# Optimization experiments

Measured on AMD Instinct MI355X. Metric: run time of the kernel, lower is better.

Reference implementation:

```python
import jax, jax.numpy as jnp
import numpy as np

B, S, DEC, ENC, ATTN = 64, 1024, 1024, 1024, 1024

def setup_inputs() -> dict:
    key = jax.random.key(0)
    k1, k2, k3, k4, k5 = jax.random.split(key, 5)
    hidden = jax.random.normal(k1, (B, DEC), dtype=jnp.float32)
    encoder_outputs = jax.random.normal(k2, (B, S, ENC), dtype=jnp.float32)
    # nn.Linear(dec+enc -> attn_dim): weight [attn, dec+enc], bias [attn]
    fan_in = DEC + ENC
    bound = 1.0 / np.sqrt(fan_in)
    W_attn = jax.random.uniform(k3, (ATTN, fan_in), dtype=jnp.float32, minval=-bound, maxval=bound)
    b_attn = jax.random.uniform(k4, (ATTN,), dtype=jnp.float32, minval=-bound, maxval=bound)
    # v = torch.rand(attn_dim) -> uniform [0,1)
    v = jax.random.uniform(k5, (ATTN,), dtype=jnp.float32)
    return {"hidden": hidden, "encoder_outputs": encoder_outputs,
            "W_attn": W_attn, "b_attn": b_attn, "v": v}

def reference(hidden, encoder_outputs, W_attn, b_attn, v):
    # hidden: [B, DEC], encoder_outputs: [B, S, ENC]
    b, s, _ = encoder_outputs.shape
    h = jnp.broadcast_to(hidden[:, None, :], (b, s, hidden.shape[-1]))
    combined = jnp.concatenate([h, encoder_outputs], axis=-1)        # [B, S, DEC+ENC]
    energy = jnp.tanh(jnp.einsum('bsf,af->bsa', combined, W_attn) + b_attn)  # [B, S, ATTN]
    scores = jnp.einsum('bsa,a->bs', energy, v)                      # [B, S]
    attn_weights = jax.nn.softmax(scores, axis=1)                    # [B, S]
    context = jnp.einsum('bs,bse->be', attn_weights, encoder_outputs)[:, None, :]  # [B, 1, ENC]
    return context
```

## Files before the change

### kernel.cpp

```cpp
#include <hip/hip_runtime.h>
#include <hip/hip_bf16.h>
#include <stdint.h>

#define NB 64
#define NS 1024
#define NE 1024
#define NA 1024
#define NF 2048
#define LDP 144

typedef __attribute__((ext_vector_type(8))) short   short8;
typedef __attribute__((ext_vector_type(4))) short   short4v;
typedef __attribute__((ext_vector_type(4))) float   f32x4;
typedef __attribute__((ext_vector_type(8))) __bf16  bf16x8;

__device__ __forceinline__ unsigned short f2bf(float x) {
  union { float f; unsigned u; } v; v.f = x;
  unsigned r = v.u + 0x7fffu + ((v.u >> 16) & 1u);
  return (unsigned short)(r >> 16);
}
__device__ __forceinline__ float bf2f(unsigned short h) {
  union { unsigned u; float f; } v; v.u = ((unsigned)h) << 16;
  return v.f;
}
__device__ __forceinline__ float tanh_fast(float x) {
  float e = __expf(2.0f * x);
  return 1.0f - __fdividef(2.0f, e + 1.0f);
}
__device__ __forceinline__ short8 pack8(float4 a, float4 b) {
  short8 h;
  h[0]=(short)f2bf(a.x); h[1]=(short)f2bf(a.y); h[2]=(short)f2bf(a.z); h[3]=(short)f2bf(a.w);
  h[4]=(short)f2bf(b.x); h[5]=(short)f2bf(b.y); h[6]=(short)f2bf(b.z); h[7]=(short)f2bf(b.w);
  return h;
}
__device__ __forceinline__ void gload_lds16(const void* g, void* l) {
  __builtin_amdgcn_global_load_lds((const __attribute__((address_space(1))) void*)g,
                                   (__attribute__((address_space(3))) void*)l, 16, 0, 0);
}

__global__ __launch_bounds__(256) void k_zero(float4* __restrict__ p, int n4) {
  int i = blockIdx.x * 256 + threadIdx.x;
  if (i < n4) { float4 z; z.x = z.y = z.z = z.w = 0.f; p[i] = z; }
}

__global__ __launch_bounds__(256) void k_conv_enc(const float4* __restrict__ src,
                                                  short8* __restrict__ dst, int n8) {
  int i = blockIdx.x * 256 + threadIdx.x;
  const int stride = gridDim.x * 256;
  for (; i < n8; i += stride) {
    float4 a = src[2 * i], b = src[2 * i + 1];
    dst[i] = pack8(a, b);
  }
}

__global__ __launch_bounds__(256) void k_conv_w(const float* __restrict__ W, short8* __restrict__ dst) {
  const int id = blockIdx.x * 256 + threadIdx.x;
  const int a = id >> 7, ku = id & 127;
  const float* s = W + (size_t)a * NF + 1024 + ku * 8;
  float4 x = *(const float4*)s;
  float4 y = *(const float4*)(s + 4);
  dst[id] = pack8(x, y);
}

__global__ __launch_bounds__(256) void k_u(const float* __restrict__ hidden,
                                           const float* __restrict__ W,
                                           const float* __restrict__ bias,
                                           float* __restrict__ u) {
  const int l = threadIdx.x & 63;
  const int w = threadIdx.x >> 6;
  const int a = (blockIdx.x >> 1) * 4 + w;
  const int bh = blockIdx.x & 1;
  const float* wrow = W + (size_t)a * NF;
  float4 wv[4];
  #pragma unroll
  for (int i = 0; i < 4; ++i) wv[i] = *(const float4*)(wrow + l * 4 + i * 256);
  const float ba = bias[a];
  for (int b = bh * 32; b < bh * 32 + 32; ++b) {
    const float* hrow = hidden + b * 1024;
    float s = 0.f;
    #pragma unroll
    for (int i = 0; i < 4; ++i) {
      float4 hv = *(const float4*)(hrow + l * 4 + i * 256);
      s += wv[i].x * hv.x + wv[i].y * hv.y + wv[i].z * hv.z + wv[i].w * hv.w;
    }
    #pragma unroll
    for (int m = 1; m < 64; m <<= 1) s += __shfl_xor(s, m);
    if (l == 0) u[b * NA + a] = s + ba;
  }
}

__global__ __launch_bounds__(512, 2) void k_main256(const unsigned short* __restrict__ Ab,
                                                    const unsigned short* __restrict__ Bb,
                                                    const float* __restrict__ u_,
                                                    const float* __restrict__ v_,
                                                    float* __restrict__ scores) {
  __shared__ __align__(16) char smem[2 * 65536];

  const int tid = threadIdx.x;
  const int l = tid & 63;
  const int w = tid >> 6;
  const int wr = w >> 2, wc = w & 3;
  const int d = blockIdx.x;
  const int xcd = d & 7, q = d >> 3;
  const int rt = xcd * 32 + (q >> 2);
  const int ct = q & 3;
  const int b = rt >> 2;
  const int lh = l >> 4, l15 = l & 15, l7 = l & 7;

  const int ssk = ((tid & 7) ^ ((tid >> 3) & 7)) * 8;
  const unsigned short* aS = Ab + (size_t)(rt * 256 + (tid >> 3)) * NE + ssk;
  const unsigned short* bS = Bb + (size_t)(ct * 256 + (tid >> 3)) * NE + ssk;
  const int wdst = w * 1024;

  f32x4 acc[8][4] = {};

#define STG2(tt, p) do { \
    char* dst_ = smem + (((tt) & 1) << 16); \
    if ((p) < 2) { \
      const unsigned short* a_ = aS + (size_t)(tt) * 64 + (size_t)(p) * 128 * NE; \
      gload_lds16(a_,                   dst_ + (p) * 128 * 128 + wdst); \
      gload_lds16(a_ + (size_t)64 * NE, dst_ + (p) * 128 * 128 + 64 * 128 + wdst); \
    } else { \
      const unsigned short* b_ = bS + (size_t)(tt) * 64 + (size_t)((p) - 2) * 128 * NE; \
      gload_lds16(b_,                   dst_ + 32768 + ((p) - 2) * 128 * 128 + wdst); \
      gload_lds16(b_ + (size_t)64 * NE, dst_ + 32768 + ((p) - 2) * 128 * 128 + 64 * 128 + wdst); \
    } } while (0)

  STG2(0, 0); STG2(0, 1); STG2(0, 2); STG2(0, 3);

  for (int t = 0; t < 16; ++t) {
    asm volatile("s_waitcnt vmcnt(0)" ::: "memory");
    asm volatile("s_barrier" ::: "memory");

    const char* As = smem + ((t & 1) << 16);
    const char* Bs = As + 32768;
    bf16x8 areg[4][2], breg[4][2];

    if (t < 15) STG2(t + 1, 0);
    #pragma unroll
    for (int rf = 0; rf < 4; ++rf)
      #pragma unroll
      for (int kh = 0; kh < 2; ++kh)
        areg[rf][kh] = *(const bf16x8*)(As + (wr * 128 + rf * 16 + l15) * 128
                                           + (((kh * 4 + lh) ^ l7) << 4));
    #pragma unroll
    for (int cf = 0; cf < 4; ++cf)
      #pragma unroll
      for (int kh = 0; kh < 2; ++kh)
        breg[cf][kh] = *(const bf16x8*)(Bs + (wc * 64 + cf * 16 + l15) * 128
                                           + (((kh * 4 + lh) ^ l7) << 4));
    __builtin_amdgcn_s_setprio(1);
    #pragma unroll
    for (int rf = 0; rf < 4; ++rf)
      #pragma unroll
      for (int cf = 0; cf < 2; ++cf)
        #pragma unroll
        for (int kh = 0; kh < 2; ++kh)
          acc[rf][cf] = __builtin_amdgcn_mfma_f32_16x16x32_bf16(areg[rf][kh], breg[cf][kh], acc[rf][cf], 0, 0, 0);
    __builtin_amdgcn_s_setprio(0);
    asm volatile("s_barrier" ::: "memory");

    if (t < 15) STG2(t + 1, 1);
    __builtin_amdgcn_s_setprio(1);
    #pragma unroll
    for (int rf = 0; rf < 4; ++rf)
      #pragma unroll
      for (int cf = 2; cf < 4; ++cf)
        #pragma unroll
        for (int kh = 0; kh < 2; ++kh)
          acc[rf][cf] = __builtin_amdgcn_mfma_f32_16x16x32_bf16(areg[rf][kh], breg[cf][kh], acc[rf][cf], 0, 0, 0);
    __builtin_amdgcn_s_setprio(0);
    asm volatile("s_barrier" ::: "memory");

    if (t < 15) STG2(t + 1, 2);
    #pragma unroll
    for (int rf = 0; rf < 4; ++rf)
      #pragma unroll
      for (int kh = 0; kh < 2; ++kh)
        areg[rf][kh] = *(const bf16x8*)(As + (wr * 128 + (4 + rf) * 16 + l15) * 128
                                           + (((kh * 4 + lh) ^ l7) << 4));
    __builtin_amdgcn_s_setprio(1);
    #pragma unroll
    for (int rf = 0; rf < 4; ++rf)
      #pragma unroll
      for (int cf = 0; cf < 2; ++cf)
        #pragma unroll
        for (int kh = 0; kh < 2; ++kh)
          acc[4 + rf][cf] = __builtin_amdgcn_mfma_f32_16x16x32_bf16(areg[rf][kh], breg[cf][kh], acc[4 + rf][cf], 0, 0, 0);
    __builtin_amdgcn_s_setprio(0);
    asm volatile("s_barrier" ::: "memory");

    if (t < 15) STG2(t + 1, 3);
    __builtin_amdgcn_s_setprio(1);
    #pragma unroll
    for (int rf = 0; rf < 4; ++rf)
      #pragma unroll
      for (int cf = 2; cf < 4; ++cf)
        #pragma unroll
        for (int kh = 0; kh < 2; ++kh)
          acc[4 + rf][cf] = __builtin_amdgcn_mfma_f32_16x16x32_bf16(areg[rf][kh], breg[cf][kh], acc[4 + rf][cf], 0, 0, 0);
    __builtin_amdgcn_s_setprio(0);
  }
#undef STG2

  const int colb = ct * 256 + wc * 64 + l15;
  float uv[4], vv[4];
  #pragma unroll
  for (int cf = 0; cf < 4; ++cf) {
    const int c = colb + cf * 16;
    uv[cf] = u_[b * NA + c];
    vv[cf] = v_[c];
  }
  #pragma unroll
  for (int rf = 0; rf < 8; ++rf) {
    #pragma unroll
    for (int reg = 0; reg < 4; ++reg) {
      float sacc = 0.f;
      #pragma unroll
      for (int cf = 0; cf < 4; ++cf)
        sacc += tanh_fast(acc[rf][cf][reg] + uv[cf]) * vv[cf];
      sacc += __shfl_xor(sacc, 1);
      sacc += __shfl_xor(sacc, 2);
      sacc += __shfl_xor(sacc, 4);
      sacc += __shfl_xor(sacc, 8);
      if (l15 == 0) {
        const int m = rt * 256 + wr * 128 + rf * 16 + lh * 4 + reg;
        atomicAdd(&scores[m], sacc);
      }
    }
  }
}

template <int ACONV, int BCONV>
__global__ __launch_bounds__(256) void k_main_rs(const void* __restrict__ Asrc,
                                                 const void* __restrict__ Bsrc,
                                                 const float* __restrict__ u_,
                                                 const float* __restrict__ v_,
                                                 float* __restrict__ scores) {
  __shared__ __align__(16) char smemf[2 * 128 * LDP];
  char* As = smemf;
  char* Bs = smemf + 128 * LDP;
  const int tid = threadIdx.x;
  const int l = tid & 63;
  const int w = tid >> 6;
  const int wr = w >> 1, wc = w & 1;
  const int d = blockIdx.x;
  const int rt = (d & 7) * 64 + (d >> 6);
  const int ct = (d >> 3) & 7;
  const int b = rt >> 3;
  const int l7 = l & 7, lh = l >> 4, l15 = l & 15;
  const int srow = w * 8 + (l >> 3);
  f32x4 acc[4][4] = {};
  for (int kt = 0; kt < 16; ++kt) {
    const int k0 = kt * 64;
    __syncthreads();
    #pragma unroll
    for (int r = 0; r < 4; ++r) {
      const int row = r * 32 + srow;
      short8 val;
      if constexpr (ACONV) {
        const float* s = (const float*)Asrc + (size_t)(rt * 128 + row) * NE + k0 + l7 * 8;
        val = pack8(*(const float4*)s, *(const float4*)(s + 4));
      } else {
        val = *(const short8*)((const unsigned short*)Asrc + (size_t)(rt * 128 + row) * NE + k0 + l7 * 8);
      }
      *(short8*)(As + row * LDP + l7 * 16) = val;
    }
    #pragma unroll
    for (int r = 0; r < 4; ++r) {
      const int row = r * 32 + srow;
      short8 val;
      if constexpr (BCONV) {
        const float* s = (const float*)Bsrc + (size_t)(ct * 128 + row) * NF + 1024 + k0 + l7 * 8;
        val = pack8(*(const float4*)s, *(const float4*)(s + 4));
      } else {
        val = *(const short8*)((const unsigned short*)Bsrc + (size_t)(ct * 128 + row) * NE + k0 + l7 * 8);
      }
      *(short8*)(Bs + row * LDP + l7 * 16) = val;
    }
    __syncthreads();
    #pragma unroll
    for (int ks = 0; ks < 2; ++ks) {
      bf16x8 af[4], bfr[4];
      const int ku = (ks * 4 + lh) * 16;
      #pragma unroll
      for (int f = 0; f < 4; ++f) {
        af[f]  = *(const bf16x8*)(As + (wr * 64 + f * 16 + l15) * LDP + ku);
        bfr[f] = *(const bf16x8*)(Bs + (wc * 64 + f * 16 + l15) * LDP + ku);
      }
      #pragma unroll
      for (int i = 0; i < 4; ++i)
        #pragma unroll
        for (int jj = 0; jj < 4; ++jj)
          acc[i][jj] = __builtin_amdgcn_mfma_f32_16x16x32_bf16(af[i], bfr[jj], acc[i][jj], 0, 0, 0);
    }
  }
  const int colb = ct * 128 + wc * 64 + l15;
  float uv[4], vv[4];
  #pragma unroll
  for (int jj = 0; jj < 4; ++jj) {
    const int c = colb + jj * 16;
    uv[jj] = u_[b * NA + c];
    vv[jj] = v_[c];
  }
  #pragma unroll
  for (int i = 0; i < 4; ++i) {
    #pragma unroll
    for (int reg = 0; reg < 4; ++reg) {
      float sacc = 0.f;
      #pragma unroll
      for (int jj = 0; jj < 4; ++jj)
        sacc += tanh_fast(acc[i][jj][reg] + uv[jj]) * vv[jj];
      sacc += __shfl_xor(sacc, 1);
      sacc += __shfl_xor(sacc, 2);
      sacc += __shfl_xor(sacc, 4);
      sacc += __shfl_xor(sacc, 8);
      if (l15 == 0) {
        const int m = rt * 128 + wr * 64 + i * 16 + lh * 4 + reg;
        atomicAdd(&scores[m], sacc);
      }
    }
  }
}

__global__ __launch_bounds__(256) void k_softmax(float* __restrict__ sc) {
  const int b = blockIdx.x, t = threadIdx.x;
  float4 x = *(float4*)(sc + b * NS + t * 4);
  float mx = fmaxf(fmaxf(x.x, x.y), fmaxf(x.z, x.w));
  #pragma unroll
  for (int m = 1; m < 64; m <<= 1) mx = fmaxf(mx, __shfl_xor(mx, m));
  __shared__ float rmax[4], rsum[4];
  if ((t & 63) == 0) rmax[t >> 6] = mx;
  __syncthreads();
  mx = fmaxf(fmaxf(rmax[0], rmax[1]), fmaxf(rmax[2], rmax[3]));
  float e0 = __expf(x.x - mx), e1 = __expf(x.y - mx);
  float e2 = __expf(x.z - mx), e3 = __expf(x.w - mx);
  float sm = e0 + e1 + e2 + e3;
  #pragma unroll
  for (int m = 1; m < 64; m <<= 1) sm += __shfl_xor(sm, m);
  if ((t & 63) == 0) rsum[t >> 6] = sm;
  __syncthreads();
  sm = rsum[0] + rsum[1] + rsum[2] + rsum[3];
  const float inv = 1.0f / sm;
  float4 o; o.x = e0 * inv; o.y = e1 * inv; o.z = e2 * inv; o.w = e3 * inv;
  *(float4*)(sc + b * NS + t * 4) = o;
}

template <int CONV>
__global__ __launch_bounds__(256) void k_ctx(const void* __restrict__ encsrc,
                                             const float* __restrict__ wgt,
                                             float* __restrict__ ctx) {
  const int b = blockIdx.x >> 4, scn = blockIdx.x & 15;
  const int t = threadIdx.x;
  float a0 = 0.f, a1 = 0.f, a2 = 0.f, a3 = 0.f;
  for (int s = scn * 64; s < scn * 64 + 64; ++s) {
    const float wv = wgt[b * NS + s];
    const size_t base = ((size_t)(b * NS + s)) * NE + t * 4;
    if constexpr (CONV) {
      float4 x = *((const float4*)((const float*)encsrc + base));
      a0 += wv * x.x; a1 += wv * x.y; a2 += wv * x.z; a3 += wv * x.w;
    } else {
      short4v hv = *(const short4v*)((const unsigned short*)encsrc + base);
      a0 += wv * bf2f((unsigned short)hv[0]);
      a1 += wv * bf2f((unsigned short)hv[1]);
      a2 += wv * bf2f((unsigned short)hv[2]);
      a3 += wv * bf2f((unsigned short)hv[3]);
    }
  }
  float* c = ctx + b * NE + t * 4;
  atomicAdd(c + 0, a0); atomicAdd(c + 1, a1);
  atomicAdd(c + 2, a2); atomicAdd(c + 3, a3);
}

__global__ __launch_bounds__(256) void k_out(const float* __restrict__ ctx,
                                             float* __restrict__ out) {
  const int i = blockIdx.x * 256 + threadIdx.x;
  float4 x = *(const float4*)(ctx + i * 4);
  *(float4*)(out + i * 4) = x;
}

extern "C" void kernel_launch(void* const* d_in, const int* in_sizes, int n_in,
                              void* d_out, int out_size, void* d_ws, size_t ws_size,
                              hipStream_t stream) {
  const float* hidden = (const float*)d_in[0];
  const float* enc    = (const float*)d_in[1];
  const float* W      = (const float*)d_in[2];
  const float* bias   = (const float*)d_in[3];
  const float* v      = (const float*)d_in[4];
  (void)in_sizes; (void)n_in; (void)out_size;

  char* ws = (char*)d_ws;
  const size_t T0 = (4ull << 20) + (128ull << 20);
  const size_t T1 = (3ull << 20);
  const int tier = (ws_size >= T0) ? 0 : ((ws_size >= T1) ? 1 : 2);

  unsigned short* Wb   = (unsigned short*)ws;
  unsigned short* encb = (unsigned short*)(ws + (4ull << 20));
  float* u_  = (tier < 2) ? (float*)(ws + (2ull << 20)) : (float*)ws;
  float* sc  = u_ + NB * NA;
  float* ctx = sc + NB * NS;

  k_u<<<512, 256, 0, stream>>>(hidden, W, bias, u_);
  k_zero<<<128, 256, 0, stream>>>((float4*)sc, (NB * NS + NB * NE) / 4);

  if (tier == 0) {
    k_conv_w<<<512, 256, 0, stream>>>(W, (short8*)Wb);
    k_conv_enc<<<2048, 256, 0, stream>>>((const float4*)enc, (short8*)encb, NB * NS * NE / 8);
    k_main256<<<1024, 512, 0, stream>>>(encb, Wb, u_, v, sc);
  } else if (tier == 1) {
    k_conv_w<<<512, 256, 0, stream>>>(W, (short8*)Wb);
    k_main_rs<1, 0><<<4096, 256, 0, stream>>>(enc, Wb, u_, v, sc);
  } else {
    k_main_rs<1, 1><<<4096, 256, 0, stream>>>(enc, W, u_, v, sc);
  }

  k_softmax<<<64, 256, 0, stream>>>(sc);
  if (tier == 0) k_ctx<0><<<1024, 256, 0, stream>>>(encb, sc, ctx);
  else           k_ctx<1><<<1024, 256, 0, stream>>>(enc, sc, ctx);
  k_out<<<64, 256, 0, stream>>>(ctx, (float*)d_out);
}
```

Measured before the change: 284.7 us.

## Prefetch two K-tiles ahead with partial vmcnt waits in GEMM main loop

The GEMM main loop now issues global-to-LDS loads for tile t+2 instead of t+1 and waits with vmcnt(8), so only the current tile's loads must have landed and one tile of loads stays in flight across iterations. B and A stages are issued as whole-tile groups after the LDS reads of the current buffer are finished, and one mid-iteration barrier is removed by splitting the B fragment reads. This aims to hide global memory latency better, but with only two LDS buffers the ordering of writes into the buffer being read depends on barrier placement, which risks races.

```diff
diff --git a/kernel.cpp b/kernel.cpp
--- a/kernel.cpp
+++ b/kernel.cpp
@@ -114,29 +114,33 @@
 
   f32x4 acc[8][4] = {};
 
-#define STG2(tt, p) do { \
+#define STG_A(tt) do { \
     char* dst_ = smem + (((tt) & 1) << 16); \
-    if ((p) < 2) { \
-      const unsigned short* a_ = aS + (size_t)(tt) * 64 + (size_t)(p) * 128 * NE; \
-      gload_lds16(a_,                   dst_ + (p) * 128 * 128 + wdst); \
-      gload_lds16(a_ + (size_t)64 * NE, dst_ + (p) * 128 * 128 + 64 * 128 + wdst); \
-    } else { \
-      const unsigned short* b_ = bS + (size_t)(tt) * 64 + (size_t)((p) - 2) * 128 * NE; \
-      gload_lds16(b_,                   dst_ + 32768 + ((p) - 2) * 128 * 128 + wdst); \
-      gload_lds16(b_ + (size_t)64 * NE, dst_ + 32768 + ((p) - 2) * 128 * 128 + 64 * 128 + wdst); \
-    } } while (0)
-
-  STG2(0, 0); STG2(0, 1); STG2(0, 2); STG2(0, 3);
+    const unsigned short* a_ = aS + (size_t)(tt) * 64; \
+    gload_lds16(a_,                    dst_ + wdst); \
+    gload_lds16(a_ + (size_t) 64 * NE, dst_ +  64 * 128 + wdst); \
+    gload_lds16(a_ + (size_t)128 * NE, dst_ + 128 * 128 + wdst); \
+    gload_lds16(a_ + (size_t)192 * NE, dst_ + 192 * 128 + wdst); } while (0)
+#define STG_B(tt) do { \
+    char* dst_ = smem + (((tt) & 1) << 16) + 32768; \
+    const unsigned short* b_ = bS + (size_t)(tt) * 64; \
+    gload_lds16(b_,                    dst_ + wdst); \
+    gload_lds16(b_ + (size_t) 64 * NE, dst_ +  64 * 128 + wdst); \
+    gload_lds16(b_ + (size_t)128 * NE, dst_ + 128 * 128 + wdst); \
+    gload_lds16(b_ + (size_t)192 * NE, dst_ + 192 * 128 + wdst); } while (0)
+
+  STG_B(0); STG_A(0); STG_B(1); STG_A(1);
+
+  bf16x8 areg[4][2], breg[4][2];
 
   for (int t = 0; t < 16; ++t) {
-    asm volatile("s_waitcnt vmcnt(0)" ::: "memory");
+    if (t < 15) asm volatile("s_waitcnt vmcnt(8)" ::: "memory");
+    else        asm volatile("s_waitcnt vmcnt(0)" ::: "memory");
     asm volatile("s_barrier" ::: "memory");
 
     const char* As = smem + ((t & 1) << 16);
     const char* Bs = As + 32768;
-    bf16x8 areg[4][2], breg[4][2];
-
-    if (t < 15) STG2(t + 1, 0);
+
     #pragma unroll
     for (int rf = 0; rf < 4; ++rf)
       #pragma unroll
@@ -144,7 +148,7 @@
         areg[rf][kh] = *(const bf16x8*)(As + (wr * 128 + rf * 16 + l15) * 128
                                            + (((kh * 4 + lh) ^ l7) << 4));
     #pragma unroll
-    for (int cf = 0; cf < 4; ++cf)
+    for (int cf = 0; cf < 2; ++cf)
       #pragma unroll
       for (int kh = 0; kh < 2; ++kh)
         breg[cf][kh] = *(const bf16x8*)(Bs + (wc * 64 + cf * 16 + l15) * 128
@@ -158,9 +162,13 @@
         for (int kh = 0; kh < 2; ++kh)
           acc[rf][cf] = __builtin_amdgcn_mfma_f32_16x16x32_bf16(areg[rf][kh], breg[cf][kh], acc[rf][cf], 0, 0, 0);
     __builtin_amdgcn_s_setprio(0);
-    asm volatile("s_barrier" ::: "memory");
-
-    if (t < 15) STG2(t + 1, 1);
+
+    #pragma unroll
+    for (int cf = 2; cf < 4; ++cf)
+      #pragma unroll
+      for (int kh = 0; kh < 2; ++kh)
+        breg[cf][kh] = *(const bf16x8*)(Bs + (wc * 64 + cf * 16 + l15) * 128
+                                           + (((kh * 4 + lh) ^ l7) << 4));
     __builtin_amdgcn_s_setprio(1);
     #pragma unroll
     for (int rf = 0; rf < 4; ++rf)
@@ -172,7 +180,7 @@
     __builtin_amdgcn_s_setprio(0);
     asm volatile("s_barrier" ::: "memory");
 
-    if (t < 15) STG2(t + 1, 2);
+    if (t < 14) STG_B(t + 2);
     #pragma unroll
     for (int rf = 0; rf < 4; ++rf)
       #pragma unroll
@@ -190,7 +198,7 @@
     __builtin_amdgcn_s_setprio(0);
     asm volatile("s_barrier" ::: "memory");
 
-    if (t < 15) STG2(t + 1, 3);
+    if (t < 14) STG_A(t + 2);
     __builtin_amdgcn_s_setprio(1);
     #pragma unroll
     for (int rf = 0; rf < 4; ++rf)
@@ -201,7 +209,8 @@
           acc[4 + rf][cf] = __builtin_amdgcn_mfma_f32_16x16x32_bf16(areg[rf][kh], breg[cf][kh], acc[4 + rf][cf], 0, 0, 0);
     __builtin_amdgcn_s_setprio(0);
   }
-#undef STG2
+#undef STG_A
+#undef STG_B
 
   const int colb = ct * 256 + wc * 64 + l15;
   float uv[4], vv[4];
```

New measurement: 281.9 us (median of 2 runs). About the same (-1.0%).
